# Kernel optimization log

Hardware: AMD Instinct MI355X
Metric: run time of the kernel (lower is better)

## Reference

```python
import jax, jax.numpy as jnp
import numpy as np

N, E, D, H, C = 20000, 320000, 128, 4, 128
NEG_SLOPE = 0.2

def _ln(x, g, b, eps=1e-5):
    mu = x.mean(-1, keepdims=True)
    var = ((x - mu) ** 2).mean(-1, keepdims=True)
    return (x - mu) * jax.lax.rsqrt(var + eps) * g + b

def _gatv2(x, src, dst, Wl, bl, Wr, br, att, b):
    # PyG GATv2Conv, concat=False (mean over heads), dropout off (eval)
    n = x.shape[0]
    xl = (x @ Wl + bl).reshape(n, H, C)   # source transform
    xr = (x @ Wr + br).reshape(n, H, C)   # destination transform
    e = jax.nn.leaky_relu(xl[src] + xr[dst], NEG_SLOPE)      # [E,H,C]
    score = jnp.einsum('ehc,hc->eh', e, att)                 # [E,H]
    m = jax.ops.segment_max(score, dst, num_segments=n)      # per-dst max
    w = jnp.exp(score - m[dst])
    denom = jax.ops.segment_sum(w, dst, num_segments=n)
    alpha = w / (denom[dst] + 1e-16)                         # softmax over incoming edges
    out = jax.ops.segment_sum(alpha[:, :, None] * xl[src], dst, num_segments=n)  # [N,H,C]
    return out.mean(axis=1) + b

def setup_inputs() -> dict:
    key = jax.random.key(0)
    ks = jax.random.split(key, 34)
    s = 1.0 / np.sqrt(D)
    def w(k, shape):
        return jax.random.normal(k, shape, jnp.float32) * s
    inp = {
        'x': jax.random.normal(ks[0], (N, D), jnp.float32),
        'edge_index': jax.random.randint(ks[1], (2, E), 0, N, jnp.int32),
        'W_in': w(ks[2], (D, C)), 'b_in': jnp.zeros((C,), jnp.float32),
        'c1_Wl': w(ks[3], (C, H * C)), 'c1_bl': jnp.zeros((H * C,), jnp.float32),
        'c1_Wr': w(ks[4], (C, H * C)), 'c1_br': jnp.zeros((H * C,), jnp.float32),
        'c1_att': w(ks[5], (H, C)), 'c1_b': jnp.zeros((C,), jnp.float32),
        'ln1_g': jnp.ones((C,), jnp.float32), 'ln1_b': jnp.zeros((C,), jnp.float32),
        'a_Wl': w(ks[6], (C, H * C)), 'a_bl': jnp.zeros((H * C,), jnp.float32),
        'a_Wr': w(ks[7], (C, H * C)), 'a_br': jnp.zeros((H * C,), jnp.float32),
        'a_att': w(ks[8], (H, C)), 'a_b': jnp.zeros((C,), jnp.float32),
        'aln_g': jnp.ones((C,), jnp.float32), 'aln_b': jnp.zeros((C,), jnp.float32),
        'ah_W': w(ks[9], (C, 1)), 'ah_b': jnp.zeros((1,), jnp.float32),
        'k_Wl': w(ks[10], (C, H * C)), 'k_bl': jnp.zeros((H * C,), jnp.float32),
        'k_Wr': w(ks[11], (C, H * C)), 'k_br': jnp.zeros((H * C,), jnp.float32),
        'k_att': w(ks[12], (H, C)), 'k_b': jnp.zeros((C,), jnp.float32),
        'kln_g': jnp.ones((C,), jnp.float32), 'kln_b': jnp.zeros((C,), jnp.float32),
        'kh_W': w(ks[13], (C, 1)), 'kh_b': jnp.zeros((1,), jnp.float32),
    }
    return inp

def reference(x, edge_index, W_in, b_in,
              c1_Wl, c1_bl, c1_Wr, c1_br, c1_att, c1_b, ln1_g, ln1_b,
              a_Wl, a_bl, a_Wr, a_br, a_att, a_b, aln_g, aln_b, ah_W, ah_b,
              k_Wl, k_bl, k_Wr, k_br, k_att, k_b, kln_g, kln_b, kh_W, kh_b):
    n = x.shape[0]
    loops = jnp.arange(n, dtype=edge_index.dtype)
    src = jnp.concatenate([edge_index[0], loops])  # PyG adds self-loops by default
    dst = jnp.concatenate([edge_index[1], loops])
    h = jax.nn.relu(x @ W_in + b_in)
    h_res = _gatv2(h, src, dst, c1_Wl, c1_bl, c1_Wr, c1_br, c1_att, c1_b)
    h = jax.nn.relu(_ln(h + h_res, ln1_g, ln1_b))
    xa = _gatv2(h, src, dst, a_Wl, a_bl, a_Wr, a_br, a_att, a_b)
    xa = jax.nn.relu(_ln(xa + h, aln_g, aln_b))
    action_logits = (xa @ ah_W + ah_b).squeeze(-1)
    xc = _gatv2(h, src, dst, k_Wl, k_bl, k_Wr, k_br, k_att, k_b)
    xc = jax.nn.relu(_ln(xc + h, kln_g, kln_b))
    state_value = xc @ kh_W + kh_b
    return action_logits, state_value
```

## Files before the change

### kernel.cpp

```cpp
#include <hip/hip_runtime.h>
#include <hip/hip_bf16.h>

typedef __hip_bfloat16 bf16;
typedef __attribute__((ext_vector_type(8))) short short8;
typedef __attribute__((ext_vector_type(4))) short short4_t;
typedef __attribute__((ext_vector_type(4))) float float4_t;
typedef __attribute__((ext_vector_type(2))) float float2v;
typedef __attribute__((ext_vector_type(2))) unsigned int uint2v;

__device__ __forceinline__ short f2bs(float f) {
    bf16 b = __float2bfloat16(f);
    return *(short*)&b;
}

template <int CTRL>
__device__ __forceinline__ float dpp_addf(float x) {
    int s = __builtin_amdgcn_update_dpp(
        0, __builtin_bit_cast(int, x), CTRL, 0xf, 0xf, true);
    return x + __builtin_bit_cast(float, s);
}
__device__ __forceinline__ float rowsum16(float x) {
    x = dpp_addf<0xB1>(x);
    x = dpp_addf<0x4E>(x);
    x = dpp_addf<0x141>(x);
    x = dpp_addf<0x140>(x);
    return x;
}

__global__ __launch_bounds__(256) void zero_kernel(int* __restrict__ a, int n) {
    int i = blockIdx.x * 256 + threadIdx.x;
    if (i < n) a[i] = 0;
}

__global__ __launch_bounds__(256) void count_kernel(const int* __restrict__ ei,
                                                    int* __restrict__ cnt, int E, int N) {
    int e = blockIdx.x * 256 + threadIdx.x;
    if (e >= E + N) return;
    int d = (e < E) ? ei[(size_t)E + e] : (e - E);
    atomicAdd(&cnt[d], 1);
}

__global__ __launch_bounds__(1024) void scan_kernel(const int* __restrict__ cnt,
                                                    int* __restrict__ rowptr, int N) {
    __shared__ int ps[1024];
    const int tid = threadIdx.x;
    const int chunk = (N + 1023) / 1024;
    const int base = tid * chunk;
    int s = 0;
    for (int i = 0; i < chunk; ++i) { int j = base + i; if (j < N) s += cnt[j]; }
    ps[tid] = s;
    __syncthreads();
    for (int off = 1; off < 1024; off <<= 1) {
        int v = (tid >= off) ? ps[tid - off] : 0;
        __syncthreads();
        ps[tid] += v;
        __syncthreads();
    }
    int run = (tid == 0) ? 0 : ps[tid - 1];
    for (int i = 0; i < chunk; ++i) {
        int j = base + i;
        if (j < N) { rowptr[j] = run; run += cnt[j]; }
    }
    if (tid == 1023) rowptr[N] = run;
}

__global__ __launch_bounds__(256) void scatter_kernel(const int* __restrict__ ei,
                                                      const int* __restrict__ rowptr,
                                                      int* __restrict__ cursor,
                                                      int* __restrict__ csr_off,
                                                      int E, int N) {
    int e = blockIdx.x * 256 + threadIdx.x;
    if (e >= E + N) return;
    int s, d;
    if (e < E) { s = ei[e]; d = ei[(size_t)E + e]; }
    else       { s = e - E; d = e - E; }
    int pos = atomicAdd(&cursor[d], 1);
    csr_off[rowptr[d] + pos] = s * 4096;
}

__global__ __launch_bounds__(256) void transpose_w_kernel(
        const float* __restrict__ W_in,
        const float* __restrict__ c1_Wl, const float* __restrict__ c1_Wr,
        const float* __restrict__ a_Wl, const float* __restrict__ a_Wr,
        const float* __restrict__ k_Wl, const float* __restrict__ k_Wr,
        bf16* __restrict__ Wt) {
    __shared__ float tile[32][33];
    const float* src; int nc, drow;
    switch (blockIdx.z) {
        case 0: src = W_in;  nc = 128; drow = 0;    break;
        case 1: src = c1_Wl; nc = 512; drow = 128;  break;
        case 2: src = c1_Wr; nc = 512; drow = 640;  break;
        case 3: src = a_Wl;  nc = 512; drow = 1152; break;
        case 4: src = a_Wr;  nc = 512; drow = 1664; break;
        case 5: src = k_Wl;  nc = 512; drow = 2176; break;
        default: src = k_Wr; nc = 512; drow = 2688; break;
    }
    const int n0 = blockIdx.x * 32;
    if (n0 >= nc) return;
    const int k0 = blockIdx.y * 32;
    const int tx = threadIdx.x & 31, ty = threadIdx.x >> 5;
#pragma unroll
    for (int i = 0; i < 4; ++i)
        tile[ty + i * 8][tx] = src[(size_t)(k0 + ty + i * 8) * nc + n0 + tx];
    __syncthreads();
#pragma unroll
    for (int i = 0; i < 4; ++i)
        Wt[(size_t)(drow + n0 + ty + i * 8) * 128 + k0 + tx] =
            __float2bfloat16(tile[tx][ty + i * 8]);
}

__global__ __launch_bounds__(256) void bias_kernel(
        const float* __restrict__ c1_bl, const float* __restrict__ c1_br,
        const float* __restrict__ a_bl, const float* __restrict__ a_br,
        const float* __restrict__ k_bl, const float* __restrict__ k_br,
        float* __restrict__ b1, float* __restrict__ bak) {
    int i = blockIdx.x * 256 + threadIdx.x;
    if (i < 1024) {
        b1[i] = (i < 512) ? c1_bl[i] : c1_br[i - 512];
    } else if (i < 3072) {
        int j = i - 1024;
        const float* b = (j < 512) ? a_bl : (j < 1024) ? a_br : (j < 1536) ? k_bl : k_br;
        bak[j] = b[j & 511];
    }
}

__global__ __launch_bounds__(256, 2) void gemm_mfma_kernel(
        const float* __restrict__ A, const bf16* __restrict__ Ab,
        const bf16* __restrict__ Wt,
        const float* __restrict__ bias,
        float* __restrict__ outF, bf16* __restrict__ outB,
        int M, int ldc, int relu) {
    __shared__ short As[128][136];
    __shared__ short Bs[128][136];
    const int tid = threadIdx.x;
    const int m0 = blockIdx.x * 128;
    const int n0 = blockIdx.y * 128;

    if (Ab) {
        short8 zero8;
#pragma unroll
        for (int q = 0; q < 8; ++q) zero8[q] = 0;
#pragma unroll
        for (int i = 0; i < 8; ++i) {
            int idx = i * 256 + tid;
            int r = idx >> 4, k8 = (idx & 15) * 8;
            int gm = m0 + r;
            short8 s = (gm < M) ? *(const short8*)&Ab[(size_t)gm * 128 + k8] : zero8;
            *(short8*)&As[r][k8] = s;
        }
    } else {
#pragma unroll
        for (int i = 0; i < 16; ++i) {
            int idx = i * 256 + tid;
            int r = idx >> 5, k4 = (idx & 31) * 4;
            int gm = m0 + r;
            float4 v = (gm < M) ? *(const float4*)&A[(size_t)gm * 128 + k4]
                                : make_float4(0.f, 0.f, 0.f, 0.f);
            short4_t s;
            s.x = f2bs(v.x); s.y = f2bs(v.y); s.z = f2bs(v.z); s.w = f2bs(v.w);
            *(short4_t*)&As[r][k4] = s;
        }
    }
#pragma unroll
    for (int i = 0; i < 8; ++i) {
        int idx = i * 256 + tid;
        int nr = idx >> 4, k8 = (idx & 15) * 8;
        *(short8*)&Bs[nr][k8] = *(const short8*)&Wt[(size_t)(n0 + nr) * 128 + k8];
    }
    __syncthreads();

    const int lane = tid & 63;
    const int w = tid >> 6;
    const int wm = (w >> 1) * 64, wn = (w & 1) * 64;
    const int fr = lane & 15;
    const int fq = (lane >> 4) * 8;

    float4_t acc[4][4] = {};
#pragma unroll
    for (int kk = 0; kk < 128; kk += 32) {
        short8 a[4], b[4];
#pragma unroll
        for (int t = 0; t < 4; ++t) a[t] = *(const short8*)&As[wm + t * 16 + fr][kk + fq];
#pragma unroll
        for (int t = 0; t < 4; ++t) b[t] = *(const short8*)&Bs[wn + t * 16 + fr][kk + fq];
#pragma unroll
        for (int ti = 0; ti < 4; ++ti)
#pragma unroll
            for (int tj = 0; tj < 4; ++tj)
                acc[ti][tj] = __builtin_amdgcn_mfma_f32_16x16x32_bf16(
                    a[ti], b[tj], acc[ti][tj], 0, 0, 0);
    }

    const int r0 = (lane >> 4) * 4;
#pragma unroll
    for (int ti = 0; ti < 4; ++ti) {
#pragma unroll
        for (int tj = 0; tj < 4; ++tj) {
            int col = n0 + wn + tj * 16 + fr;
            float bz = bias[col];
#pragma unroll
            for (int r = 0; r < 4; ++r) {
                size_t row = m0 + wm + ti * 16 + r0 + r;
                float v = acc[ti][tj][r] + bz;
                if (relu) v = fmaxf(v, 0.f);
                if (outF) outF[row * ldc + col] = v;
                if (outB) outB[row * ldc + col] = __float2bfloat16(v);
            }
        }
    }
}

__global__ __launch_bounds__(256) void gat_kernel(
        const bf16* __restrict__ xl, const bf16* __restrict__ xr,
        const float* __restrict__ att,
        const int* __restrict__ rowptr, const int* __restrict__ csr_off,
        const float* __restrict__ h_res,
        const float* __restrict__ gbias,
        const float* __restrict__ ln_g, const float* __restrict__ ln_b,
        float* __restrict__ h_out, bf16* __restrict__ h_outb,
        const float* __restrict__ head_W, const float* __restrict__ head_b,
        float* __restrict__ out_scalar, int mode) {
    const int n = blockIdx.x;
    const int tid = threadIdx.x;
    const int h = tid >> 6;
    const int lane = tid & 63;
    const int g = lane >> 4;
    const int sl = lane & 15;
    const int cb = sl * 8;

    float2v c1[4], c2[4], xr2[4];
    {
        const float* ap = att + h * 128 + cb;
        short8 v = *(const short8*)(xr + (size_t)n * 2048 + h * 128 + cb);
        const unsigned int* uv = (const unsigned int*)&v;
#pragma unroll
        for (int j = 0; j < 4; ++j) {
            float a0 = ap[2 * j], a1 = ap[2 * j + 1];
            c1[j].x = 0.6f * a0; c1[j].y = 0.6f * a1;
            c2[j].x = 0.4f * a0; c2[j].y = 0.4f * a1;
            unsigned u = uv[j];
            xr2[j].x = __uint_as_float(u << 16);
            xr2[j].y = __uint_as_float(u & 0xffff0000u);
        }
    }
    const int rs = rowptr[n], re = rowptr[n + 1];
    const int nit = (re - rs + 3) >> 2;
    const int self = n * 4096;
    const char* xlh = (const char*)xl + (size_t)(h * 128 + cb) * 2;

    float l = 0.f;
    float2v acc2[4] = {};
    int e = rs + g;
    int o2 = (e + 8 < re) ? csr_off[e + 8] : self;
    short8 va = *(const short8*)(xlh + ((e < re) ? csr_off[e] : self));
    short8 vb = *(const short8*)(xlh + ((e + 4 < re) ? csr_off[e + 4] : self));

    for (int it = 0; it < nit; ++it, e += 4) {
        const bool valid = (e < re);
        short8 vc = va;
        va = vb;
        if (e + 8 < re) {
            vb = *(const short8*)(xlh + o2);
            o2 = (e + 12 < re) ? csr_off[e + 12] : self;
        }
        const unsigned int* uv = (const unsigned int*)&vc;
        float2v pa = {0.f, 0.f}, pb = {0.f, 0.f};
        float2v xs[4];
#pragma unroll
        for (int j = 0; j < 4; ++j) {
            unsigned u = uv[j];
            float2v x;
            x.x = __uint_as_float(u << 16);
            x.y = __uint_as_float(u & 0xffff0000u);
            xs[j] = x;
            float2v t = x + xr2[j];
            float2v ta = __builtin_bit_cast(float2v,
                           __builtin_bit_cast(uint2v, t) & 0x7fffffffu);
            pa = __builtin_elementwise_fma(c1[j], t, pa);
            pb = __builtin_elementwise_fma(c2[j], ta, pb);
        }
        float p = rowsum16((pa.x + pb.x) + (pa.y + pb.y));
        p = valid ? fminf(p, 60.f) : -1e30f;
        float wv = __expf(p);
        l += wv;
        float2v ws = {wv, wv};
#pragma unroll
        for (int j = 0; j < 4; ++j)
            acc2[j] = __builtin_elementwise_fma(ws, xs[j], acc2[j]);
    }
    float* accf = (float*)acc2;
#pragma unroll
    for (int off = 16; off <= 32; off <<= 1) {
        l += __shfl_xor(l, off, 64);
#pragma unroll
        for (int j = 0; j < 8; ++j) accf[j] += __shfl_xor(accf[j], off, 64);
    }
    const float inv = 0.25f / (l + 1e-16f);

    __shared__ float sm[4][128];
    __shared__ float red[8];
    if (g == 0) {
#pragma unroll
        for (int j = 0; j < 8; ++j) sm[h][cb + j] = accf[j] * inv;
    }
    __syncthreads();

    float v = 0.f;
    if (tid < 128)
        v = sm[0][tid] + sm[1][tid] + sm[2][tid] + sm[3][tid]
          + gbias[tid] + h_res[(size_t)n * 128 + tid];
    float s1 = rowsum16(v), s2 = rowsum16(v * v);
    s1 += __shfl_xor(s1, 16, 64); s2 += __shfl_xor(s2, 16, 64);
    s1 += __shfl_xor(s1, 32, 64); s2 += __shfl_xor(s2, 32, 64);
    if (lane == 0) { red[h] = s1; red[4 + h] = s2; }
    __syncthreads();
    const float mu   = (red[0] + red[1] + red[2] + red[3]) * 0.0078125f;
    const float var  = (red[4] + red[5] + red[6] + red[7]) * 0.0078125f - mu * mu;
    const float rstd = rsqrtf(var + 1e-5f);
    float y = 0.f;
    if (tid < 128) {
        y = fmaf((v - mu) * rstd, ln_g[tid], ln_b[tid]);
        y = fmaxf(y, 0.f);
    }
    if (mode == 0) {
        if (tid < 128) {
            h_out[(size_t)n * 128 + tid] = y;
            h_outb[(size_t)n * 128 + tid] = __float2bfloat16(y);
        }
    } else {
        float d = (tid < 128) ? y * head_W[tid] : 0.f;
        d = rowsum16(d);
        d += __shfl_xor(d, 16, 64);
        d += __shfl_xor(d, 32, 64);
        __syncthreads();
        if (lane == 0) red[h] = d;
        __syncthreads();
        if (tid == 0) out_scalar[n] = red[0] + red[1] + red[2] + red[3] + head_b[0];
    }
}

extern "C" void kernel_launch(void* const* d_in, const int* in_sizes, int n_in,
                              void* d_out, int out_size, void* d_ws, size_t ws_size,
                              hipStream_t stream) {
    const float* x      = (const float*)d_in[0];
    const int*   ei     = (const int*)  d_in[1];
    const float* W_in   = (const float*)d_in[2];
    const float* b_in   = (const float*)d_in[3];
    const float* c1_Wl  = (const float*)d_in[4];
    const float* c1_bl  = (const float*)d_in[5];
    const float* c1_Wr  = (const float*)d_in[6];
    const float* c1_br  = (const float*)d_in[7];
    const float* c1_att = (const float*)d_in[8];
    const float* c1_b   = (const float*)d_in[9];
    const float* ln1_g  = (const float*)d_in[10];
    const float* ln1_b  = (const float*)d_in[11];
    const float* a_Wl   = (const float*)d_in[12];
    const float* a_bl   = (const float*)d_in[13];
    const float* a_Wr   = (const float*)d_in[14];
    const float* a_br   = (const float*)d_in[15];
    const float* a_att  = (const float*)d_in[16];
    const float* a_b    = (const float*)d_in[17];
    const float* aln_g  = (const float*)d_in[18];
    const float* aln_b  = (const float*)d_in[19];
    const float* ah_W   = (const float*)d_in[20];
    const float* ah_b   = (const float*)d_in[21];
    const float* k_Wl   = (const float*)d_in[22];
    const float* k_bl   = (const float*)d_in[23];
    const float* k_Wr   = (const float*)d_in[24];
    const float* k_br   = (const float*)d_in[25];
    const float* k_att  = (const float*)d_in[26];
    const float* k_b    = (const float*)d_in[27];
    const float* kln_g  = (const float*)d_in[28];
    const float* kln_b  = (const float*)d_in[29];
    const float* kh_W   = (const float*)d_in[30];
    const float* kh_b   = (const float*)d_in[31];

    const int N  = in_sizes[0] / 128;
    const int E  = in_sizes[1] / 2;
    const int ET = E + N;
    const int MB = (N + 127) / 128;
    const int Npad = MB * 128;

    char* ws = (char*)d_ws;
    size_t off = 0;
    auto alloc = [&](size_t bytes) -> void* {
        void* p = ws + off;
        off += (bytes + 255) & ~(size_t)255;
        return p;
    };
    int*   rowptr  = (int*)alloc((size_t)(N + 1) * 4);
    int*   cntcur  = (int*)alloc((size_t)2 * N * 4);
    int*   csr_off = (int*)alloc((size_t)ET * 4);
    float* h0      = (float*)alloc((size_t)Npad * 128 * 4);
    bf16*  h0b     = (bf16*)alloc((size_t)Npad * 128 * 2);
    float* h1      = (float*)alloc((size_t)Npad * 128 * 4);
    bf16*  h1b     = (bf16*)alloc((size_t)Npad * 128 * 2);
    bf16*  Wt      = (bf16*)alloc((size_t)3200 * 128 * 2);
    float* b1cat   = (float*)alloc(1024 * 4);
    float* bakcat  = (float*)alloc(2048 * 4);
    bf16*  cat     = (bf16*)alloc((size_t)Npad * 2048 * 2);

    int* cnt    = cntcur;
    int* cursor = cntcur + N;
    const bf16* Wt_in = Wt;
    const bf16* Wt_1  = Wt + 128 * 128;
    const bf16* Wt_ak = Wt + 128 * 128 + 1024 * 128;

    float* out_logits = (float*)d_out;
    float* out_value  = (float*)d_out + N;

    zero_kernel<<<(2 * N + 255) / 256, 256, 0, stream>>>(cntcur, 2 * N);
    count_kernel<<<(ET + 255) / 256, 256, 0, stream>>>(ei, cnt, E, N);
    transpose_w_kernel<<<dim3(16, 4, 7), 256, 0, stream>>>(
        W_in, c1_Wl, c1_Wr, a_Wl, a_Wr, k_Wl, k_Wr, Wt);
    bias_kernel<<<12, 256, 0, stream>>>(c1_bl, c1_br, a_bl, a_br, k_bl, k_br, b1cat, bakcat);
    scan_kernel<<<1, 1024, 0, stream>>>(cnt, rowptr, N);
    scatter_kernel<<<(ET + 255) / 256, 256, 0, stream>>>(ei, rowptr, cursor, csr_off, E, N);

    gemm_mfma_kernel<<<dim3(MB, 1), 256, 0, stream>>>(x, nullptr, Wt_in, b_in,
                                                      h0, h0b, N, 128, 1);
    gemm_mfma_kernel<<<dim3(MB, 8), 256, 0, stream>>>(nullptr, h0b, Wt_1, b1cat,
                                                      nullptr, cat, Npad, 2048, 0);
    gat_kernel<<<N, 256, 0, stream>>>(cat, cat + 512, c1_att, rowptr, csr_off,
                                      h0, c1_b, ln1_g, ln1_b, h1, h1b,
                                      nullptr, nullptr, nullptr, 0);
    gemm_mfma_kernel<<<dim3(MB, 16), 256, 0, stream>>>(nullptr, h1b, Wt_ak, bakcat,
                                                       nullptr, cat, Npad, 2048, 0);
    gat_kernel<<<N, 256, 0, stream>>>(cat, cat + 512, a_att, rowptr, csr_off,
                                      h1, a_b, aln_g, aln_b, nullptr, nullptr,
                                      ah_W, ah_b, out_logits, 1);
    gat_kernel<<<N, 256, 0, stream>>>(cat + 1024, cat + 1536, k_att, rowptr, csr_off,
                                      h1, k_b, kln_g, kln_b, nullptr, nullptr,
                                      kh_W, kh_b, out_value, 1);
}
```

Baseline: 439.2 us.

## Map one wavefront per destination node with all heads, removing block sync

The GAT kernel changes from one 256-thread block per node (one wave per head, four edge groups) to one wave per node. Each 16-lane group now handles one head and walks every incoming edge sequentially, with a two-deep prefetch. Head averaging becomes cross-lane shuffles, and LayerNorm and the head dot product run inside 16 lanes, so shared memory and __syncthreads are gone. The aim is to cut synchronisation and idle lanes on low-degree nodes, at the cost of fewer edges in flight per node, which can stretch latency for high-degree nodes.

```diff
diff --git a/kernel.cpp b/kernel.cpp
--- a/kernel.cpp
+++ b/kernel.cpp
@@ -219,19 +219,17 @@
         const float* __restrict__ ln_g, const float* __restrict__ ln_b,
         float* __restrict__ h_out, bf16* __restrict__ h_outb,
         const float* __restrict__ head_W, const float* __restrict__ head_b,
-        float* __restrict__ out_scalar, int mode) {
-    const int n = blockIdx.x;
-    const int tid = threadIdx.x;
-    const int h = tid >> 6;
-    const int lane = tid & 63;
-    const int g = lane >> 4;
+        float* __restrict__ out_scalar, int mode, int N) {
+    const int n = blockIdx.x * 4 + (threadIdx.x >> 6);
+    if (n >= N) return;
+    const int lane = threadIdx.x & 63;
     const int sl = lane & 15;
-    const int cb = sl * 8;
+    const int hc = (lane >> 4) * 128 + sl * 8;
 
     float2v c1[4], c2[4], xr2[4];
     {
-        const float* ap = att + h * 128 + cb;
-        short8 v = *(const short8*)(xr + (size_t)n * 2048 + h * 128 + cb);
+        const float* ap = att + hc;
+        short8 v = *(const short8*)(xr + (size_t)n * 2048 + hc);
         const unsigned int* uv = (const unsigned int*)&v;
 #pragma unroll
         for (int j = 0; j < 4; ++j) {
@@ -244,26 +242,23 @@
         }
     }
     const int rs = rowptr[n], re = rowptr[n + 1];
-    const int nit = (re - rs + 3) >> 2;
-    const int self = n * 4096;
-    const char* xlh = (const char*)xl + (size_t)(h * 128 + cb) * 2;
+    const char* xlh = (const char*)xl + (size_t)hc * 2;
 
     float l = 0.f;
     float2v acc2[4] = {};
-    int e = rs + g;
-    int o2 = (e + 8 < re) ? csr_off[e + 8] : self;
-    short8 va = *(const short8*)(xlh + ((e < re) ? csr_off[e] : self));
-    short8 vb = *(const short8*)(xlh + ((e + 4 < re) ? csr_off[e + 4] : self));
-
-    for (int it = 0; it < nit; ++it, e += 4) {
-        const bool valid = (e < re);
-        short8 vc = va;
-        va = vb;
-        if (e + 8 < re) {
+    int o0 = csr_off[rs];
+    short8 va = *(const short8*)(xlh + o0);
+    int o1 = (rs + 1 < re) ? csr_off[rs + 1] : o0;
+    short8 vb = *(const short8*)(xlh + o1);
+    int o2 = (rs + 2 < re) ? csr_off[rs + 2] : o0;
+
+    for (int e = rs; e < re; ++e) {
+        short8 cur = va; va = vb;
+        if (e + 2 < re) {
             vb = *(const short8*)(xlh + o2);
-            o2 = (e + 12 < re) ? csr_off[e + 12] : self;
-        }
-        const unsigned int* uv = (const unsigned int*)&vc;
+            o2 = (e + 3 < re) ? csr_off[e + 3] : o0;
+        }
+        const unsigned int* uv = (const unsigned int*)&cur;
         float2v pa = {0.f, 0.f}, pb = {0.f, 0.f};
         float2v xs[4];
 #pragma unroll
@@ -280,62 +275,58 @@
             pb = __builtin_elementwise_fma(c2[j], ta, pb);
         }
         float p = rowsum16((pa.x + pb.x) + (pa.y + pb.y));
-        p = valid ? fminf(p, 60.f) : -1e30f;
-        float wv = __expf(p);
+        float wv = __expf(fminf(p, 60.f));
         l += wv;
         float2v ws = {wv, wv};
 #pragma unroll
         for (int j = 0; j < 4; ++j)
             acc2[j] = __builtin_elementwise_fma(ws, xs[j], acc2[j]);
     }
+
     float* accf = (float*)acc2;
-#pragma unroll
-    for (int off = 16; off <= 32; off <<= 1) {
-        l += __shfl_xor(l, off, 64);
+    const float inv = 0.25f / (l + 1e-16f);
+#pragma unroll
+    for (int j = 0; j < 8; ++j) accf[j] *= inv;
+#pragma unroll
+    for (int off = 16; off <= 32; off <<= 1)
 #pragma unroll
         for (int j = 0; j < 8; ++j) accf[j] += __shfl_xor(accf[j], off, 64);
-    }
-    const float inv = 0.25f / (l + 1e-16f);
-
-    __shared__ float sm[4][128];
-    __shared__ float red[8];
-    if (g == 0) {
-#pragma unroll
-        for (int j = 0; j < 8; ++j) sm[h][cb + j] = accf[j] * inv;
-    }
-    __syncthreads();
-
-    float v = 0.f;
-    if (tid < 128)
-        v = sm[0][tid] + sm[1][tid] + sm[2][tid] + sm[3][tid]
-          + gbias[tid] + h_res[(size_t)n * 128 + tid];
-    float s1 = rowsum16(v), s2 = rowsum16(v * v);
-    s1 += __shfl_xor(s1, 16, 64); s2 += __shfl_xor(s2, 16, 64);
-    s1 += __shfl_xor(s1, 32, 64); s2 += __shfl_xor(s2, 32, 64);
-    if (lane == 0) { red[h] = s1; red[4 + h] = s2; }
-    __syncthreads();
-    const float mu   = (red[0] + red[1] + red[2] + red[3]) * 0.0078125f;
-    const float var  = (red[4] + red[5] + red[6] + red[7]) * 0.0078125f - mu * mu;
-    const float rstd = rsqrtf(var + 1e-5f);
-    float y = 0.f;
-    if (tid < 128) {
-        y = fmaf((v - mu) * rstd, ln_g[tid], ln_b[tid]);
-        y = fmaxf(y, 0.f);
-    }
-    if (mode == 0) {
-        if (tid < 128) {
-            h_out[(size_t)n * 128 + tid] = y;
-            h_outb[(size_t)n * 128 + tid] = __float2bfloat16(y);
-        }
-    } else {
-        float d = (tid < 128) ? y * head_W[tid] : 0.f;
-        d = rowsum16(d);
-        d += __shfl_xor(d, 16, 64);
-        d += __shfl_xor(d, 32, 64);
-        __syncthreads();
-        if (lane == 0) red[h] = d;
-        __syncthreads();
-        if (tid == 0) out_scalar[n] = red[0] + red[1] + red[2] + red[3] + head_b[0];
+
+    if (lane < 16) {
+        const int cb = sl * 8;
+        const float* hr = h_res + (size_t)n * 128 + cb;
+        float vv[8];
+#pragma unroll
+        for (int j = 0; j < 8; ++j) vv[j] = accf[j] + gbias[cb + j] + hr[j];
+        float t1 = 0.f, t2 = 0.f;
+#pragma unroll
+        for (int j = 0; j < 8; ++j) { t1 += vv[j]; t2 += vv[j] * vv[j]; }
+        const float s1 = rowsum16(t1), s2 = rowsum16(t2);
+        const float mu   = s1 * 0.0078125f;
+        const float var  = s2 * 0.0078125f - mu * mu;
+        const float rstd = rsqrtf(var + 1e-5f);
+        float y[8];
+#pragma unroll
+        for (int j = 0; j < 8; ++j) {
+            y[j] = fmaf((vv[j] - mu) * rstd, ln_g[cb + j], ln_b[cb + j]);
+            y[j] = fmaxf(y[j], 0.f);
+        }
+        if (mode == 0) {
+            float4 y0 = make_float4(y[0], y[1], y[2], y[3]);
+            float4 y1 = make_float4(y[4], y[5], y[6], y[7]);
+            *(float4*)(h_out + (size_t)n * 128 + cb) = y0;
+            *(float4*)(h_out + (size_t)n * 128 + cb + 4) = y1;
+            short8 yb;
+#pragma unroll
+            for (int j = 0; j < 8; ++j) yb[j] = f2bs(y[j]);
+            *(short8*)(h_outb + (size_t)n * 128 + cb) = yb;
+        } else {
+            float d = 0.f;
+#pragma unroll
+            for (int j = 0; j < 8; ++j) d += y[j] * head_W[cb + j];
+            d = rowsum16(d);
+            if (lane == 0) out_scalar[n] = d + head_b[0];
+        }
     }
 }
 
@@ -421,15 +412,15 @@
                                                       h0, h0b, N, 128, 1);
     gemm_mfma_kernel<<<dim3(MB, 8), 256, 0, stream>>>(nullptr, h0b, Wt_1, b1cat,
                                                       nullptr, cat, Npad, 2048, 0);
-    gat_kernel<<<N, 256, 0, stream>>>(cat, cat + 512, c1_att, rowptr, csr_off,
+    gat_kernel<<<(N + 3) / 4, 256, 0, stream>>>(cat, cat + 512, c1_att, rowptr, csr_off,
                                       h0, c1_b, ln1_g, ln1_b, h1, h1b,
-                                      nullptr, nullptr, nullptr, 0);
+                                      nullptr, nullptr, nullptr, 0, N);
     gemm_mfma_kernel<<<dim3(MB, 16), 256, 0, stream>>>(nullptr, h1b, Wt_ak, bakcat,
                                                        nullptr, cat, Npad, 2048, 0);
-    gat_kernel<<<N, 256, 0, stream>>>(cat, cat + 512, a_att, rowptr, csr_off,
+    gat_kernel<<<(N + 3) / 4, 256, 0, stream>>>(cat, cat + 512, a_att, rowptr, csr_off,
                                       h1, a_b, aln_g, aln_b, nullptr, nullptr,
-                                      ah_W, ah_b, out_logits, 1);
-    gat_kernel<<<N, 256, 0, stream>>>(cat + 1024, cat + 1536, k_att, rowptr, csr_off,
+                                      ah_W, ah_b, out_logits, 1, N);
+    gat_kernel<<<(N + 3) / 4, 256, 0, stream>>>(cat + 1024, cat + 1536, k_att, rowptr, csr_off,
                                       h1, k_b, kln_g, kln_b, nullptr, nullptr,
-                                      kh_W, kh_b, out_value, 1);
-}
+                                      kh_W, kh_b, out_value, 1, N);
+}
```

Measured after the change: 419.6 us. 4.5% less time.
